# Optimization experiments

Hardware: AMD Instinct MI355X
Metric: run time of the kernel (lower is better)

The kernel has to match this reference:

```python
import jax, jax.numpy as jnp
import numpy as np

MAX_K = 16
CLUSTER_ITERS = 3
TEMP = 0.8
EPS = 1e-6


def setup_inputs() -> dict:
    key = jax.random.key(0)
    k1, k2 = jax.random.split(key, 2)
    B, C, H, W = 4, 256, 128, 128
    embeddings = jax.random.normal(k1, (B, C, H, W), dtype=jnp.float32)
    # 1x1 conv == per-pixel linear: weight [max_k, C], bias [max_k]
    seed_w = jax.random.normal(k2, (MAX_K, C), dtype=jnp.float32) * 0.05
    seed_b = jnp.zeros((MAX_K,), dtype=jnp.float32)
    return {"embeddings": embeddings, "seed_w": seed_w, "seed_b": seed_b, "k": 8}


def reference(embeddings, seed_w, seed_b, k):
    b, c, h, w = embeddings.shape
    n = h * w
    feats = embeddings.reshape(b, c, n)                     # [b,c,n]

    # seed_proj (1x1 conv) restricted to first k output channels
    seeds = jnp.einsum('oc,bcn->bon', seed_w[:k], feats) + seed_b[:k][None, :, None]
    assign = jax.nn.softmax(seeds, axis=1)                  # [b,k,n]
    proto = jnp.einsum('bkn,bcn->bkc', assign, feats) / (assign.sum(axis=2)[..., None] + EPS)

    # ||f||^2 is constant across iterations
    f_sq = jnp.sum(feats * feats, axis=1)                   # [b,n]

    logits = None
    for _ in range(CLUSTER_ITERS):                          # small fixed iter count
        p_sq = jnp.sum(proto * proto, axis=2)               # [b,k]
        cross = jnp.einsum('bkc,bcn->bkn', proto, feats)    # [b,k,n]
        # squared L2 distance via matmul trick (same math as (f-p)^2 sum over c)
        dist = f_sq[:, None, :] + p_sq[:, :, None] - 2.0 * cross
        logits = -dist / TEMP                               # [b,k,n]
        assign = jax.nn.softmax(logits, axis=1)
        denom = assign.sum(axis=2, keepdims=True) + EPS     # [b,k,1]
        proto = jnp.einsum('bkn,bcn->bkc', assign, feats) / denom

    logits_map = logits.reshape(b, k, h, w)
    probs = jax.nn.softmax(logits_map, axis=1)
    # bilinear upsample x4, align_corners=False (half-pixel) == jax 'linear' resize
    probs_full = jax.image.resize(probs, (b, k, 4 * h, 4 * w), method='linear')
    return probs_full, proto, logits_map
```

## Files before the change

kernel.cpp:

```cpp
#include <hip/hip_runtime.h>
#include <hip/hip_bf16.h>
#include <math.h>

#define BB   4
#define CCH  256
#define KK   8
#define NPIX 16384
#define TILE 64
#define NBLK 256
#define TEMP_INV 1.25f
#define EPSF 1e-6f

__device__ __forceinline__ float bf_lo(unsigned int u) { return __uint_as_float(u << 16); }
__device__ __forceinline__ float bf_hi(unsigned int u) { return __uint_as_float(u & 0xffff0000u); }

template<int MODE>
__global__ __launch_bounds__(512, 6)
void skm_pass(const float* __restrict__ feats,
              const float* __restrict__ seed_w,
              const float* __restrict__ seed_b,
              const float* __restrict__ proto_t,
              const float* __restrict__ psq_ws,
              float* __restrict__ fsq,
              float* __restrict__ part_num,
              float* __restrict__ part_den,
              float* __restrict__ logits_out,
              float* __restrict__ probs_out)
{
    __shared__ unsigned int fb_s[CCH][32];
    __shared__ float cross_s[8][KK][66];
    __shared__ float w_s[KK][68];
    __shared__ float aux_s[8][TILE];

    const int t   = threadIdx.x;
    const int bid = blockIdx.x;
    const int b   = bid >> 8;
    const int blk = bid & 255;
    const int n0  = blk * TILE;

    const int p  = t & 63;
    const int g  = t >> 6;
    const int c0 = __builtin_amdgcn_readfirstlane(g) * 32;
    const float* fcol = feats + (size_t)b * CCH * NPIX + (size_t)c0 * NPIX + n0 + p;
    const float* pt   = proto_t + (size_t)b * CCH * KK + (size_t)c0 * KK;

    float cr[KK];
    #pragma unroll
    for (int k = 0; k < KK; ++k) cr[k] = 0.f;
    float fs = 0.f;

    #pragma unroll 8
    for (int cc = 0; cc < 32; ++cc) {
        const float f = fcol[(size_t)cc * NPIX];
        if (MODE == 0) fs = fmaf(f, f, fs);
        const int c  = c0 + cc;
        const int wp = (p >> 1) ^ ((c & 15) << 1);
        ((__hip_bfloat16*)fb_s)[(c << 6) + (wp << 1) + (p & 1)] = __float2bfloat16(f);
        if (MODE == 0) {
            #pragma unroll
            for (int k = 0; k < KK; ++k)
                cr[k] = fmaf(seed_w[k * CCH + c], f, cr[k]);
        } else {
            const float* pr = pt + cc * KK;
            #pragma unroll
            for (int k = 0; k < KK; ++k)
                cr[k] = fmaf(pr[k], f, cr[k]);
        }
    }
    #pragma unroll
    for (int k = 0; k < KK; ++k) cross_s[g][k][p] = cr[k];
    if (MODE == 0) aux_s[g][p] = fs;
    __syncthreads();

    {
        const int pp = t >> 3, k = t & 7;
        float lg = 0.f;
        #pragma unroll
        for (int gg = 0; gg < 8; ++gg) lg += cross_s[gg][k][pp];
        if (MODE == 0) {
            lg += seed_b[k];
            if (k == 0) {
                float fv = 0.f;
                #pragma unroll
                for (int gg = 0; gg < 8; ++gg) fv += aux_s[gg][pp];
                fsq[b * NPIX + n0 + pp] = fv;
            }
        } else {
            const float fv = fsq[b * NPIX + n0 + pp];
            const float pk = psq_ws[b * KK + k];
            lg = (2.f * lg - fv - pk) * TEMP_INV;
        }
        float m = lg;
        m = fmaxf(m, __shfl_xor(m, 1, 64));
        m = fmaxf(m, __shfl_xor(m, 2, 64));
        m = fmaxf(m, __shfl_xor(m, 4, 64));
        const float e = expf(lg - m);
        float ssum = e;
        ssum += __shfl_xor(ssum, 1, 64);
        ssum += __shfl_xor(ssum, 2, 64);
        ssum += __shfl_xor(ssum, 4, 64);
        const float wv = e / ssum;
        w_s[k][pp] = wv;
        if (MODE == 2) aux_s[k][pp] = lg;
    }
    __syncthreads();

    if (MODE == 2) {
        const int k2 = t >> 6, p2 = t & 63;
        logits_out[((size_t)b * KK + k2) * NPIX + n0 + p2] = aux_s[k2][p2];
        probs_out [((size_t)b * KK + k2) * NPIX + n0 + p2] = w_s[k2][p2];
    }

    if (t < 256) {
        const int kk = t >> 5, l = t & 31;
        float s = w_s[kk][2 * l] + w_s[kk][2 * l + 1];
        s += __shfl_xor(s, 16, 64);
        s += __shfl_xor(s, 8, 64);
        s += __shfl_xor(s, 4, 64);
        s += __shfl_xor(s, 2, 64);
        s += __shfl_xor(s, 1, 64);
        if (l == 0) part_den[(b * NBLK + blk) * KK + kk] = s;
    }

    {
        const int c = t & 255, h = t >> 8;
        const int s2 = (c & 15) << 1;
        const uint2* row2 = (const uint2*)fb_s[c];
        float acc[KK];
        #pragma unroll
        for (int k = 0; k < KK; ++k) acc[k] = 0.f;
        #pragma unroll
        for (int j = 0; j < 8; ++j) {
            const uint2 u = row2[((16 * h + 2 * j) ^ s2) >> 1];
            const float f0 = bf_lo(u.x), f1 = bf_hi(u.x);
            const float f2 = bf_lo(u.y), f3 = bf_hi(u.y);
            const int px = 32 * h + 4 * j;
            #pragma unroll
            for (int k = 0; k < KK; ++k) {
                const float4 w4 = *(const float4*)&w_s[k][px];
                acc[k] = fmaf(f3, w4.w, fmaf(f2, w4.z,
                         fmaf(f1, w4.y, fmaf(f0, w4.x, acc[k]))));
            }
        }
        float (*acc_s)[KK][CCH] = (float (*)[KK][CCH])cross_s;
        #pragma unroll
        for (int k = 0; k < KK; ++k) acc_s[h][k][c] = acc[k];
        __syncthreads();
        #pragma unroll
        for (int u2 = t; u2 < KK * CCH; u2 += 512) {
            const int k = u2 >> 8, c2 = u2 & 255;
            part_num[(((size_t)b * NBLK + blk) * KK + k) * CCH + c2] =
                acc_s[0][k][c2] + acc_s[1][k][c2];
        }
    }
}

__global__ __launch_bounds__(1024)
void skm_reduce(const float* __restrict__ part_num,
                const float* __restrict__ part_den,
                float* __restrict__ proto_t,
                float* __restrict__ psq_ws,
                float* __restrict__ proto_out)
{
    const int bid = blockIdx.x;
    const int b = bid >> 3, k = bid & 7;
    const int t = threadIdx.x;
    const int jj = t >> 8, c = t & 255;

    float s = 0.f;
    #pragma unroll 8
    for (int j = 0; j < 64; ++j)
        s += part_num[(((size_t)b * NBLK + jj * 64 + j) * KK + k) * CCH + c];

    __shared__ float red_s[4][CCH];
    __shared__ float den4[4];
    __shared__ float red2[CCH];
    red_s[jj][c] = s;

    if (t < 256) {
        float dv = part_den[(b * NBLK + t) * KK + k];
        dv += __shfl_xor(dv, 32, 64);
        dv += __shfl_xor(dv, 16, 64);
        dv += __shfl_xor(dv, 8, 64);
        dv += __shfl_xor(dv, 4, 64);
        dv += __shfl_xor(dv, 2, 64);
        dv += __shfl_xor(dv, 1, 64);
        if ((t & 63) == 0) den4[t >> 6] = dv;
    }
    __syncthreads();

    if (t < 256) {
        const float den = den4[0] + den4[1] + den4[2] + den4[3] + EPSF;
        const float pv = (red_s[0][t] + red_s[1][t] + red_s[2][t] + red_s[3][t]) / den;
        proto_t[((size_t)b * CCH + t) * KK + k] = pv;
        if (proto_out) proto_out[(b * KK + k) * CCH + t] = pv;
        red2[t] = pv * pv;
    }
    __syncthreads();
    if (t < 64) {
        float v = red2[t] + red2[t + 64] + red2[t + 128] + red2[t + 192];
        v += __shfl_xor(v, 32, 64);
        v += __shfl_xor(v, 16, 64);
        v += __shfl_xor(v, 8, 64);
        v += __shfl_xor(v, 4, 64);
        v += __shfl_xor(v, 2, 64);
        v += __shfl_xor(v, 1, 64);
        if (t == 0) psq_ws[b * KK + k] = v;
    }
}

__global__ __launch_bounds__(256)
void skm_upsample(const float* __restrict__ probs, float* __restrict__ outp)
{
    const int gid = blockIdx.x * 256 + threadIdx.x;
    const int jb = gid & 127;
    const int i  = (gid >> 7) & 511;
    const int bk = gid >> 16;
    const float* src = probs + (size_t)bk * NPIX;

    const float y   = i * 0.25f - 0.375f;
    const float y0f = floorf(y);
    const float fy  = y - y0f;
    const int   y0  = (int)y0f;
    const int ya = min(max(y0, 0), 127);
    const int yb = min(max(y0 + 1, 0), 127);
    const int xm = max(jb - 1, 0);
    const int xp = min(jb + 1, 127);

    const float* r0 = src + ya * 128;
    const float* r1 = src + yb * 128;
    const float wy0 = 1.f - fy;
    const float am = r0[xm] * wy0 + r1[xm] * fy;
    const float ac = r0[jb] * wy0 + r1[jb] * fy;
    const float ap = r0[xp] * wy0 + r1[xp] * fy;

    float4 o;
    o.x = 0.375f * am + 0.625f * ac;
    o.y = 0.125f * am + 0.875f * ac;
    o.z = 0.875f * ac + 0.125f * ap;
    o.w = 0.625f * ac + 0.375f * ap;
    ((float4*)outp)[gid] = o;
}

extern "C" void kernel_launch(void* const* d_in, const int* in_sizes, int n_in,
                              void* d_out, int out_size, void* d_ws, size_t ws_size,
                              hipStream_t stream)
{
    const float* feats  = (const float*)d_in[0];
    const float* seed_w = (const float*)d_in[1];
    const float* seed_b = (const float*)d_in[2];

    float* out        = (float*)d_out;
    float* probs_full = out;
    float* proto_out  = out + 8388608;
    float* logits_out = out + 8388608 + 8192;

    float* part_num = probs_full;

    float* ws       = (float*)d_ws;
    float* fsq      = ws;
    float* part_den = ws + 65536;
    float* proto_t  = part_den + 8192;
    float* psq_ws   = proto_t + 8192;
    float* probs_ws = psq_ws + 32;

    const dim3 pg(BB * NBLK), pb(512);
    const dim3 rg(32), rb(1024);

    skm_pass<0><<<pg, pb, 0, stream>>>(feats, seed_w, seed_b, proto_t, psq_ws,
                                       fsq, part_num, part_den, nullptr, nullptr);
    skm_reduce<<<rg, rb, 0, stream>>>(part_num, part_den, proto_t, psq_ws, nullptr);
    skm_pass<1><<<pg, pb, 0, stream>>>(feats, seed_w, seed_b, proto_t, psq_ws,
                                       fsq, part_num, part_den, nullptr, nullptr);
    skm_reduce<<<rg, rb, 0, stream>>>(part_num, part_den, proto_t, psq_ws, nullptr);
    skm_pass<1><<<pg, pb, 0, stream>>>(feats, seed_w, seed_b, proto_t, psq_ws,
                                       fsq, part_num, part_den, nullptr, nullptr);
    skm_reduce<<<rg, rb, 0, stream>>>(part_num, part_den, proto_t, psq_ws, nullptr);
    skm_pass<2><<<pg, pb, 0, stream>>>(feats, seed_w, seed_b, proto_t, psq_ws,
                                       fsq, part_num, part_den, logits_out, probs_ws);
    skm_reduce<<<rg, rb, 0, stream>>>(part_num, part_den, proto_t, psq_ws, proto_out);
    skm_upsample<<<dim3(8192), dim3(256), 0, stream>>>(probs_ws, probs_full);
}
```

Before: 109.6 us.

## Cache bf16 feature copy for later passes, split reduce, fuse upsample

The first pass writes a bf16 copy of the features to workspace, and later passes read it instead of the fp32 input, halving feature read traffic. The reduce kernel is split into 288 smaller blocks per (batch, cluster), with channel slices reduced separately. The final reduce launch also carries the upsample blocks, removing one launch. The cost is an extra 32MB write in pass 0 and bf16 rounding of the cross-term in later iterations, which changes numerics. It also needs a large workspace and falls back to the old path otherwise.

New measurement: 177.5 us. +62.0%, slower.

```diff
diff --git a/kernel.cpp b/kernel.cpp
--- a/kernel.cpp
+++ b/kernel.cpp
@@ -11,10 +11,12 @@
 #define TEMP_INV 1.25f
 #define EPSF 1e-6f
 
+typedef unsigned short ushort_t;
+
 __device__ __forceinline__ float bf_lo(unsigned int u) { return __uint_as_float(u << 16); }
 __device__ __forceinline__ float bf_hi(unsigned int u) { return __uint_as_float(u & 0xffff0000u); }
 
-template<int MODE>
+template<int MODE, int BF>
 __global__ __launch_bounds__(512, 6)
 void skm_pass(const float* __restrict__ feats,
               const float* __restrict__ seed_w,
@@ -25,7 +27,8 @@
               float* __restrict__ part_num,
               float* __restrict__ part_den,
               float* __restrict__ logits_out,
-              float* __restrict__ probs_out)
+              float* __restrict__ probs_out,
+              __hip_bfloat16* __restrict__ feats_bf)
 {
     __shared__ unsigned int fb_s[CCH][32];
     __shared__ float cross_s[8][KK][66];
@@ -38,38 +41,65 @@
     const int blk = bid & 255;
     const int n0  = blk * TILE;
 
-    const int p  = t & 63;
-    const int g  = t >> 6;
-    const int c0 = __builtin_amdgcn_readfirstlane(g) * 32;
-    const float* fcol = feats + (size_t)b * CCH * NPIX + (size_t)c0 * NPIX + n0 + p;
-    const float* pt   = proto_t + (size_t)b * CCH * KK + (size_t)c0 * KK;
-
-    float cr[KK];
-    #pragma unroll
-    for (int k = 0; k < KK; ++k) cr[k] = 0.f;
-    float fs = 0.f;
-
-    #pragma unroll 8
-    for (int cc = 0; cc < 32; ++cc) {
-        const float f = fcol[(size_t)cc * NPIX];
-        if (MODE == 0) fs = fmaf(f, f, fs);
-        const int c  = c0 + cc;
-        const int wp = (p >> 1) ^ ((c & 15) << 1);
-        ((__hip_bfloat16*)fb_s)[(c << 6) + (wp << 1) + (p & 1)] = __float2bfloat16(f);
-        if (MODE == 0) {
-            #pragma unroll
-            for (int k = 0; k < KK; ++k)
-                cr[k] = fmaf(seed_w[k * CCH + c], f, cr[k]);
-        } else {
+    const int l   = t & 63;
+    const int g   = t >> 6;
+    const int c0g = __builtin_amdgcn_readfirstlane(g) * 32;
+
+    if (MODE == 0 || !BF) {
+        const int p = l;
+        const float* fcol = feats + (size_t)b * CCH * NPIX + (size_t)c0g * NPIX + n0 + p;
+        const float* pt   = proto_t + (size_t)b * CCH * KK + (size_t)c0g * KK;
+        float cr[KK];
+        #pragma unroll
+        for (int k = 0; k < KK; ++k) cr[k] = 0.f;
+        float fs = 0.f;
+        #pragma unroll 8
+        for (int cc = 0; cc < 32; ++cc) {
+            const float f = fcol[(size_t)cc * NPIX];
+            if (MODE == 0) fs = fmaf(f, f, fs);
+            const int c  = c0g + cc;
+            const int wp = (p >> 1) ^ ((c & 15) << 1);
+            const __hip_bfloat16 hv = __float2bfloat16(f);
+            ((__hip_bfloat16*)fb_s)[(c << 6) + (wp << 1) + (p & 1)] = hv;
+            if (MODE == 0 && BF)
+                feats_bf[(size_t)(b * CCH + c) * NPIX + n0 + p] = hv;
+            if (MODE == 0) {
+                #pragma unroll
+                for (int k = 0; k < KK; ++k)
+                    cr[k] = fmaf(seed_w[k * CCH + c], f, cr[k]);
+            } else {
+                const float* pr = pt + cc * KK;
+                #pragma unroll
+                for (int k = 0; k < KK; ++k)
+                    cr[k] = fmaf(pr[k], f, cr[k]);
+            }
+        }
+        #pragma unroll
+        for (int k = 0; k < KK; ++k) cross_s[g][k][p] = cr[k];
+        if (MODE == 0) aux_s[g][p] = fs;
+    } else {
+        const int wsel = l & 31;
+        const int sh   = (l < 32) ? 16 : 0;
+        const int p1   = 2 * wsel + (l >> 5);
+        const ushort_t* fbrow = (const ushort_t*)feats_bf
+                              + (size_t)(b * CCH + c0g) * NPIX + n0 + 2 * wsel;
+        const float* pt = proto_t + (size_t)b * CCH * KK + (size_t)c0g * KK;
+        float cr[KK];
+        #pragma unroll
+        for (int k = 0; k < KK; ++k) cr[k] = 0.f;
+        #pragma unroll 8
+        for (int cc = 0; cc < 32; ++cc) {
+            const unsigned int u = *(const unsigned int*)(fbrow + (size_t)cc * NPIX);
+            const float f = __uint_as_float((u << sh) & 0xffff0000u);
+            if (l < 32) fb_s[c0g + cc][wsel ^ ((cc & 15) << 1)] = u;
             const float* pr = pt + cc * KK;
             #pragma unroll
             for (int k = 0; k < KK; ++k)
                 cr[k] = fmaf(pr[k], f, cr[k]);
         }
-    }
-    #pragma unroll
-    for (int k = 0; k < KK; ++k) cross_s[g][k][p] = cr[k];
-    if (MODE == 0) aux_s[g][p] = fs;
+        #pragma unroll
+        for (int k = 0; k < KK; ++k) cross_s[g][k][p1] = cr[k];
+    }
     __syncthreads();
 
     {
@@ -112,14 +142,14 @@
     }
 
     if (t < 256) {
-        const int kk = t >> 5, l = t & 31;
-        float s = w_s[kk][2 * l] + w_s[kk][2 * l + 1];
+        const int kk = t >> 5, ll = t & 31;
+        float s = w_s[kk][2 * ll] + w_s[kk][2 * ll + 1];
         s += __shfl_xor(s, 16, 64);
         s += __shfl_xor(s, 8, 64);
         s += __shfl_xor(s, 4, 64);
         s += __shfl_xor(s, 2, 64);
         s += __shfl_xor(s, 1, 64);
-        if (l == 0) part_den[(b * NBLK + blk) * KK + kk] = s;
+        if (ll == 0) part_den[(b * NBLK + blk) * KK + kk] = s;
     }
 
     {
@@ -155,57 +185,104 @@
     }
 }
 
-__global__ __launch_bounds__(1024)
+template<bool FINAL>
+__global__ __launch_bounds__(256)
 void skm_reduce(const float* __restrict__ part_num,
                 const float* __restrict__ part_den,
                 float* __restrict__ proto_t,
                 float* __restrict__ psq_ws,
-                float* __restrict__ proto_out)
+                float* __restrict__ proto_out,
+                const float* __restrict__ probs_ws,
+                float* __restrict__ probs_full)
 {
     const int bid = blockIdx.x;
-    const int b = bid >> 3, k = bid & 7;
+    if (FINAL && bid >= 288) {
+        const int gid = (bid - 288) * 256 + threadIdx.x;
+        const int jb = gid & 127;
+        const int i  = (gid >> 7) & 511;
+        const int bk = gid >> 16;
+        const float* src = probs_ws + (size_t)bk * NPIX;
+        const float y   = i * 0.25f - 0.375f;
+        const float y0f = floorf(y);
+        const float fy  = y - y0f;
+        const int   y0  = (int)y0f;
+        const int ya = min(max(y0, 0), 127);
+        const int yb = min(max(y0 + 1, 0), 127);
+        const int xm = max(jb - 1, 0);
+        const int xp = min(jb + 1, 127);
+        const float* r0 = src + ya * 128;
+        const float* r1 = src + yb * 128;
+        const float wy0 = 1.f - fy;
+        const float am = r0[xm] * wy0 + r1[xm] * fy;
+        const float ac = r0[jb] * wy0 + r1[jb] * fy;
+        const float ap = r0[xp] * wy0 + r1[xp] * fy;
+        float4 o;
+        o.x = 0.375f * am + 0.625f * ac;
+        o.y = 0.125f * am + 0.875f * ac;
+        o.z = 0.875f * ac + 0.125f * ap;
+        o.w = 0.625f * ac + 0.375f * ap;
+        ((float4*)probs_full)[gid] = o;
+        return;
+    }
+
+    const int cq = bid % 9;
+    const int bk = bid / 9;
+    const int b = bk >> 3, k = bk & 7;
     const int t = threadIdx.x;
-    const int jj = t >> 8, c = t & 255;
-
-    float s = 0.f;
-    #pragma unroll 8
-    for (int j = 0; j < 64; ++j)
-        s += part_num[(((size_t)b * NBLK + jj * 64 + j) * KK + k) * CCH + c];
-
-    __shared__ float red_s[4][CCH];
-    __shared__ float den4[4];
-    __shared__ float red2[CCH];
-    red_s[jj][c] = s;
-
-    if (t < 256) {
-        float dv = part_den[(b * NBLK + t) * KK + k];
-        dv += __shfl_xor(dv, 32, 64);
-        dv += __shfl_xor(dv, 16, 64);
-        dv += __shfl_xor(dv, 8, 64);
-        dv += __shfl_xor(dv, 4, 64);
-        dv += __shfl_xor(dv, 2, 64);
-        dv += __shfl_xor(dv, 1, 64);
-        if ((t & 63) == 0) den4[t >> 6] = dv;
-    }
+
+    __shared__ float red[8][32];
+    __shared__ float den_s[4];
+    __shared__ float red2[256];
+
+    float dv = part_den[(b * NBLK + t) * KK + k];
+    dv += __shfl_xor(dv, 32, 64);
+    dv += __shfl_xor(dv, 16, 64);
+    dv += __shfl_xor(dv, 8, 64);
+    dv += __shfl_xor(dv, 4, 64);
+    dv += __shfl_xor(dv, 2, 64);
+    dv += __shfl_xor(dv, 1, 64);
+    if ((t & 63) == 0) den_s[t >> 6] = dv;
     __syncthreads();
-
-    if (t < 256) {
-        const float den = den4[0] + den4[1] + den4[2] + den4[3] + EPSF;
-        const float pv = (red_s[0][t] + red_s[1][t] + red_s[2][t] + red_s[3][t]) / den;
-        proto_t[((size_t)b * CCH + t) * KK + k] = pv;
-        if (proto_out) proto_out[(b * KK + k) * CCH + t] = pv;
+    const float den = den_s[0] + den_s[1] + den_s[2] + den_s[3] + EPSF;
+
+    if (cq < 8) {
+        const int jj = t >> 5, cl = t & 31;
+        const int c = cq * 32 + cl;
+        float s = 0.f;
+        #pragma unroll 4
+        for (int j = 0; j < 32; ++j)
+            s += part_num[(((size_t)b * NBLK + jj * 32 + j) * KK + k) * CCH + c];
+        red[jj][cl] = s;
+        __syncthreads();
+        if (t < 32) {
+            float pv = 0.f;
+            #pragma unroll
+            for (int j2 = 0; j2 < 8; ++j2) pv += red[j2][t];
+            pv /= den;
+            const int c2 = cq * 32 + t;
+            proto_t[((size_t)b * CCH + c2) * KK + k] = pv;
+            if (proto_out) proto_out[(b * KK + k) * CCH + c2] = pv;
+        }
+    } else {
+        float num = 0.f;
+        #pragma unroll 8
+        for (int j = 0; j < NBLK; ++j)
+            num += part_num[(((size_t)b * NBLK + j) * KK + k) * CCH + t];
+        const float pv = num / den;
         red2[t] = pv * pv;
-    }
-    __syncthreads();
-    if (t < 64) {
-        float v = red2[t] + red2[t + 64] + red2[t + 128] + red2[t + 192];
-        v += __shfl_xor(v, 32, 64);
-        v += __shfl_xor(v, 16, 64);
-        v += __shfl_xor(v, 8, 64);
-        v += __shfl_xor(v, 4, 64);
-        v += __shfl_xor(v, 2, 64);
-        v += __shfl_xor(v, 1, 64);
-        if (t == 0) psq_ws[b * KK + k] = v;
+        __syncthreads();
+        if (t < 128) red2[t] += red2[t + 128];
+        __syncthreads();
+        if (t < 64) {
+            float v = red2[t] + red2[t + 64];
+            v += __shfl_xor(v, 32, 64);
+            v += __shfl_xor(v, 16, 64);
+            v += __shfl_xor(v, 8, 64);
+            v += __shfl_xor(v, 4, 64);
+            v += __shfl_xor(v, 2, 64);
+            v += __shfl_xor(v, 1, 64);
+            if (t == 0) psq_ws[b * KK + k] = v;
+        }
     }
 }
 
@@ -217,7 +294,6 @@
     const int i  = (gid >> 7) & 511;
     const int bk = gid >> 16;
     const float* src = probs + (size_t)bk * NPIX;
-
     const float y   = i * 0.25f - 0.375f;
     const float y0f = floorf(y);
     const float fy  = y - y0f;
@@ -226,14 +302,12 @@
     const int yb = min(max(y0 + 1, 0), 127);
     const int xm = max(jb - 1, 0);
     const int xp = min(jb + 1, 127);
-
     const float* r0 = src + ya * 128;
     const float* r1 = src + yb * 128;
     const float wy0 = 1.f - fy;
     const float am = r0[xm] * wy0 + r1[xm] * fy;
     const float ac = r0[jb] * wy0 + r1[jb] * fy;
     const float ap = r0[xp] * wy0 + r1[xp] * fy;
-
     float4 o;
     o.x = 0.375f * am + 0.625f * ac;
     o.y = 0.125f * am + 0.875f * ac;
@@ -255,8 +329,6 @@
     float* proto_out  = out + 8388608;
     float* logits_out = out + 8388608 + 8192;
 
-    float* part_num = probs_full;
-
     float* ws       = (float*)d_ws;
     float* fsq      = ws;
     float* part_den = ws + 65536;
@@ -264,20 +336,48 @@
     float* psq_ws   = proto_t + 8192;
     float* probs_ws = psq_ws + 32;
 
+    const bool big_ws = ws_size >= (size_t)45 * 1024 * 1024;
+    __hip_bfloat16* feats_bf = (__hip_bfloat16*)(ws + 606272);
+    float* part_num = big_ws ? (ws + 606272 + 16777216)
+                             : probs_full;
+
     const dim3 pg(BB * NBLK), pb(512);
-    const dim3 rg(32), rb(1024);
-
-    skm_pass<0><<<pg, pb, 0, stream>>>(feats, seed_w, seed_b, proto_t, psq_ws,
-                                       fsq, part_num, part_den, nullptr, nullptr);
-    skm_reduce<<<rg, rb, 0, stream>>>(part_num, part_den, proto_t, psq_ws, nullptr);
-    skm_pass<1><<<pg, pb, 0, stream>>>(feats, seed_w, seed_b, proto_t, psq_ws,
-                                       fsq, part_num, part_den, nullptr, nullptr);
-    skm_reduce<<<rg, rb, 0, stream>>>(part_num, part_den, proto_t, psq_ws, nullptr);
-    skm_pass<1><<<pg, pb, 0, stream>>>(feats, seed_w, seed_b, proto_t, psq_ws,
-                                       fsq, part_num, part_den, nullptr, nullptr);
-    skm_reduce<<<rg, rb, 0, stream>>>(part_num, part_den, proto_t, psq_ws, nullptr);
-    skm_pass<2><<<pg, pb, 0, stream>>>(feats, seed_w, seed_b, proto_t, psq_ws,
-                                       fsq, part_num, part_den, logits_out, probs_ws);
-    skm_reduce<<<rg, rb, 0, stream>>>(part_num, part_den, proto_t, psq_ws, proto_out);
-    skm_upsample<<<dim3(8192), dim3(256), 0, stream>>>(probs_ws, probs_full);
+    const dim3 rg(288), rb(256);
+
+    if (big_ws) {
+        skm_pass<0,1><<<pg, pb, 0, stream>>>(feats, seed_w, seed_b, proto_t, psq_ws,
+                                             fsq, part_num, part_den, nullptr, nullptr, feats_bf);
+        skm_reduce<false><<<rg, rb, 0, stream>>>(part_num, part_den, proto_t, psq_ws,
+                                                 nullptr, probs_ws, probs_full);
+        skm_pass<1,1><<<pg, pb, 0, stream>>>(feats, seed_w, seed_b, proto_t, psq_ws,
+                                             fsq, part_num, part_den, nullptr, nullptr, feats_bf);
+        skm_reduce<false><<<rg, rb, 0, stream>>>(part_num, part_den, proto_t, psq_ws,
+                                                 nullptr, probs_ws, probs_full);
+        skm_pass<1,1><<<pg, pb, 0, stream>>>(feats, seed_w, seed_b, proto_t, psq_ws,
+                                             fsq, part_num, part_den, nullptr, nullptr, feats_bf);
+        skm_reduce<false><<<rg, rb, 0, stream>>>(part_num, part_den, proto_t, psq_ws,
+                                                 nullptr, probs_ws, probs_full);
+        skm_pass<2,1><<<pg, pb, 0, stream>>>(feats, seed_w, seed_b, proto_t, psq_ws,
+                                             fsq, part_num, part_den, logits_out, probs_ws, feats_bf);
+        skm_reduce<true><<<dim3(288 + 8192), rb, 0, stream>>>(part_num, part_den, proto_t, psq_ws,
+                                                              proto_out, probs_ws, probs_full);
+    } else {
+        skm_pass<0,0><<<pg, pb, 0, stream>>>(feats, seed_w, seed_b, proto_t, psq_ws,
+                                             fsq, part_num, part_den, nullptr, nullptr, nullptr);
+        skm_reduce<false><<<rg, rb, 0, stream>>>(part_num, part_den, proto_t, psq_ws,
+                                                 nullptr, probs_ws, probs_full);
+        skm_pass<1,0><<<pg, pb, 0, stream>>>(feats, seed_w, seed_b, proto_t, psq_ws,
+                                             fsq, part_num, part_den, nullptr, nullptr, nullptr);
+        skm_reduce<false><<<rg, rb, 0, stream>>>(part_num, part_den, proto_t, psq_ws,
+                                                 nullptr, probs_ws, probs_full);
+        skm_pass<1,0><<<pg, pb, 0, stream>>>(feats, seed_w, seed_b, proto_t, psq_ws,
+                                             fsq, part_num, part_den, nullptr, nullptr, nullptr);
+        skm_reduce<false><<<rg, rb, 0, stream>>>(part_num, part_den, proto_t, psq_ws,
+                                                 nullptr, probs_ws, probs_full);
+        skm_pass<2,0><<<pg, pb, 0, stream>>>(feats, seed_w, seed_b, proto_t, psq_ws,
+                                             fsq, part_num, part_den, logits_out, probs_ws, nullptr);
+        skm_reduce<false><<<rg, rb, 0, stream>>>(part_num, part_den, proto_t, psq_ws,
+                                                 proto_out, probs_ws, probs_full);
+        skm_upsample<<<dim3(8192), dim3(256), 0, stream>>>(probs_ws, probs_full);
+    }
 }
```

## Split prototype reduction across more blocks and fuse upsample into final reduce

Applied to the files above, without the earlier changes.

The prototype reduction now runs as 288 blocks of 256 threads instead of 32 blocks of 1024. Each (b,k) gets eight channel-slice blocks plus one block that recomputes the full sum only to get the squared prototype norm, which spreads the partial-sum reads over more CUs. The final reduce launch also carries the bilinear upsample blocks, removing one kernel launch. Partial numerators move from the output buffer into workspace, which is needed because the upsample now writes the output concurrently. The price is duplicated reading of partials by the norm blocks.

Result: slower. 140.1 us (+27.9%).

```diff
diff --git a/kernel.cpp b/kernel.cpp
--- a/kernel.cpp
+++ b/kernel.cpp
@@ -112,14 +112,14 @@
     }
 
     if (t < 256) {
-        const int kk = t >> 5, l = t & 31;
-        float s = w_s[kk][2 * l] + w_s[kk][2 * l + 1];
+        const int kk = t >> 5, ll = t & 31;
+        float s = w_s[kk][2 * ll] + w_s[kk][2 * ll + 1];
         s += __shfl_xor(s, 16, 64);
         s += __shfl_xor(s, 8, 64);
         s += __shfl_xor(s, 4, 64);
         s += __shfl_xor(s, 2, 64);
         s += __shfl_xor(s, 1, 64);
-        if (l == 0) part_den[(b * NBLK + blk) * KK + kk] = s;
+        if (ll == 0) part_den[(b * NBLK + blk) * KK + kk] = s;
     }
 
     {
@@ -155,91 +155,105 @@
     }
 }
 
-__global__ __launch_bounds__(1024)
+template<bool FINAL>
+__global__ __launch_bounds__(256)
 void skm_reduce(const float* __restrict__ part_num,
                 const float* __restrict__ part_den,
                 float* __restrict__ proto_t,
                 float* __restrict__ psq_ws,
-                float* __restrict__ proto_out)
+                float* __restrict__ proto_out,
+                const float* __restrict__ probs_ws,
+                float* __restrict__ probs_full)
 {
     const int bid = blockIdx.x;
-    const int b = bid >> 3, k = bid & 7;
+    if (FINAL && bid >= 288) {
+        const int gid = (bid - 288) * 256 + threadIdx.x;
+        const int jb = gid & 127;
+        const int i  = (gid >> 7) & 511;
+        const int bk = gid >> 16;
+        const float* src = probs_ws + (size_t)bk * NPIX;
+        const float y   = i * 0.25f - 0.375f;
+        const float y0f = floorf(y);
+        const float fy  = y - y0f;
+        const int   y0  = (int)y0f;
+        const int ya = min(max(y0, 0), 127);
+        const int yb = min(max(y0 + 1, 0), 127);
+        const int xm = max(jb - 1, 0);
+        const int xp = min(jb + 1, 127);
+        const float* r0 = src + ya * 128;
+        const float* r1 = src + yb * 128;
+        const float wy0 = 1.f - fy;
+        const float am = r0[xm] * wy0 + r1[xm] * fy;
+        const float ac = r0[jb] * wy0 + r1[jb] * fy;
+        const float ap = r0[xp] * wy0 + r1[xp] * fy;
+        float4 o;
+        o.x = 0.375f * am + 0.625f * ac;
+        o.y = 0.125f * am + 0.875f * ac;
+        o.z = 0.875f * ac + 0.125f * ap;
+        o.w = 0.625f * ac + 0.375f * ap;
+        ((float4*)probs_full)[gid] = o;
+        return;
+    }
+
+    const int cq = bid % 9;
+    const int bk = bid / 9;
+    const int b = bk >> 3, k = bk & 7;
     const int t = threadIdx.x;
-    const int jj = t >> 8, c = t & 255;
-
-    float s = 0.f;
-    #pragma unroll 8
-    for (int j = 0; j < 64; ++j)
-        s += part_num[(((size_t)b * NBLK + jj * 64 + j) * KK + k) * CCH + c];
-
-    __shared__ float red_s[4][CCH];
-    __shared__ float den4[4];
-    __shared__ float red2[CCH];
-    red_s[jj][c] = s;
-
-    if (t < 256) {
-        float dv = part_den[(b * NBLK + t) * KK + k];
-        dv += __shfl_xor(dv, 32, 64);
-        dv += __shfl_xor(dv, 16, 64);
-        dv += __shfl_xor(dv, 8, 64);
-        dv += __shfl_xor(dv, 4, 64);
-        dv += __shfl_xor(dv, 2, 64);
-        dv += __shfl_xor(dv, 1, 64);
-        if ((t & 63) == 0) den4[t >> 6] = dv;
-    }
+
+    __shared__ float red[8][32];
+    __shared__ float den_s[4];
+    __shared__ float red2[256];
+
+    float dv = part_den[(b * NBLK + t) * KK + k];
+    dv += __shfl_xor(dv, 32, 64);
+    dv += __shfl_xor(dv, 16, 64);
+    dv += __shfl_xor(dv, 8, 64);
+    dv += __shfl_xor(dv, 4, 64);
+    dv += __shfl_xor(dv, 2, 64);
+    dv += __shfl_xor(dv, 1, 64);
+    if ((t & 63) == 0) den_s[t >> 6] = dv;
     __syncthreads();
-
-    if (t < 256) {
-        const float den = den4[0] + den4[1] + den4[2] + den4[3] + EPSF;
-        const float pv = (red_s[0][t] + red_s[1][t] + red_s[2][t] + red_s[3][t]) / den;
-        proto_t[((size_t)b * CCH + t) * KK + k] = pv;
-        if (proto_out) proto_out[(b * KK + k) * CCH + t] = pv;
+    const float den = den_s[0] + den_s[1] + den_s[2] + den_s[3] + EPSF;
+
+    if (cq < 8) {
+        const int jj = t >> 5, cl = t & 31;
+        const int c = cq * 32 + cl;
+        float s = 0.f;
+        #pragma unroll 4
+        for (int j = 0; j < 32; ++j)
+            s += part_num[(((size_t)b * NBLK + jj * 32 + j) * KK + k) * CCH + c];
+        red[jj][cl] = s;
+        __syncthreads();
+        if (t < 32) {
+            float pv = 0.f;
+            #pragma unroll
+            for (int j2 = 0; j2 < 8; ++j2) pv += red[j2][t];
+            pv /= den;
+            const int c2 = cq * 32 + t;
+            proto_t[((size_t)b * CCH + c2) * KK + k] = pv;
+            if (proto_out) proto_out[(b * KK + k) * CCH + c2] = pv;
+        }
+    } else {
+        float num = 0.f;
+        #pragma unroll 8
+        for (int j = 0; j < NBLK; ++j)
+            num += part_num[(((size_t)b * NBLK + j) * KK + k) * CCH + t];
+        const float pv = num / den;
         red2[t] = pv * pv;
-    }
-    __syncthreads();
-    if (t < 64) {
-        float v = red2[t] + red2[t + 64] + red2[t + 128] + red2[t + 192];
-        v += __shfl_xor(v, 32, 64);
-        v += __shfl_xor(v, 16, 64);
-        v += __shfl_xor(v, 8, 64);
-        v += __shfl_xor(v, 4, 64);
-        v += __shfl_xor(v, 2, 64);
-        v += __shfl_xor(v, 1, 64);
-        if (t == 0) psq_ws[b * KK + k] = v;
-    }
-}
-
-__global__ __launch_bounds__(256)
-void skm_upsample(const float* __restrict__ probs, float* __restrict__ outp)
-{
-    const int gid = blockIdx.x * 256 + threadIdx.x;
-    const int jb = gid & 127;
-    const int i  = (gid >> 7) & 511;
-    const int bk = gid >> 16;
-    const float* src = probs + (size_t)bk * NPIX;
-
-    const float y   = i * 0.25f - 0.375f;
-    const float y0f = floorf(y);
-    const float fy  = y - y0f;
-    const int   y0  = (int)y0f;
-    const int ya = min(max(y0, 0), 127);
-    const int yb = min(max(y0 + 1, 0), 127);
-    const int xm = max(jb - 1, 0);
-    const int xp = min(jb + 1, 127);
-
-    const float* r0 = src + ya * 128;
-    const float* r1 = src + yb * 128;
-    const float wy0 = 1.f - fy;
-    const float am = r0[xm] * wy0 + r1[xm] * fy;
-    const float ac = r0[jb] * wy0 + r1[jb] * fy;
-    const float ap = r0[xp] * wy0 + r1[xp] * fy;
-
-    float4 o;
-    o.x = 0.375f * am + 0.625f * ac;
-    o.y = 0.125f * am + 0.875f * ac;
-    o.z = 0.875f * ac + 0.125f * ap;
-    o.w = 0.625f * ac + 0.375f * ap;
-    ((float4*)outp)[gid] = o;
+        __syncthreads();
+        if (t < 128) red2[t] += red2[t + 128];
+        __syncthreads();
+        if (t < 64) {
+            float v = red2[t] + red2[t + 64];
+            v += __shfl_xor(v, 32, 64);
+            v += __shfl_xor(v, 16, 64);
+            v += __shfl_xor(v, 8, 64);
+            v += __shfl_xor(v, 4, 64);
+            v += __shfl_xor(v, 2, 64);
+            v += __shfl_xor(v, 1, 64);
+            if (t == 0) psq_ws[b * KK + k] = v;
+        }
+    }
 }
 
 extern "C" void kernel_launch(void* const* d_in, const int* in_sizes, int n_in,
@@ -255,29 +269,31 @@
     float* proto_out  = out + 8388608;
     float* logits_out = out + 8388608 + 8192;
 
-    float* part_num = probs_full;
-
     float* ws       = (float*)d_ws;
     float* fsq      = ws;
     float* part_den = ws + 65536;
     float* proto_t  = part_den + 8192;
     float* psq_ws   = proto_t + 8192;
     float* probs_ws = psq_ws + 32;
+    float* part_num = probs_ws + 524288;
 
     const dim3 pg(BB * NBLK), pb(512);
-    const dim3 rg(32), rb(1024);
+    const dim3 rg(288), rb(256);
 
     skm_pass<0><<<pg, pb, 0, stream>>>(feats, seed_w, seed_b, proto_t, psq_ws,
                                        fsq, part_num, part_den, nullptr, nullptr);
-    skm_reduce<<<rg, rb, 0, stream>>>(part_num, part_den, proto_t, psq_ws, nullptr);
+    skm_reduce<false><<<rg, rb, 0, stream>>>(part_num, part_den, proto_t, psq_ws,
+                                             nullptr, probs_ws, probs_full);
     skm_pass<1><<<pg, pb, 0, stream>>>(feats, seed_w, seed_b, proto_t, psq_ws,
                                        fsq, part_num, part_den, nullptr, nullptr);
-    skm_reduce<<<rg, rb, 0, stream>>>(part_num, part_den, proto_t, psq_ws, nullptr);
+    skm_reduce<false><<<rg, rb, 0, stream>>>(part_num, part_den, proto_t, psq_ws,
+                                             nullptr, probs_ws, probs_full);
     skm_pass<1><<<pg, pb, 0, stream>>>(feats, seed_w, seed_b, proto_t, psq_ws,
                                        fsq, part_num, part_den, nullptr, nullptr);
-    skm_reduce<<<rg, rb, 0, stream>>>(part_num, part_den, proto_t, psq_ws, nullptr);
+    skm_reduce<false><<<rg, rb, 0, stream>>>(part_num, part_den, proto_t, psq_ws,
+                                             nullptr, probs_ws, probs_full);
     skm_pass<2><<<pg, pb, 0, stream>>>(feats, seed_w, seed_b, proto_t, psq_ws,
                                        fsq, part_num, part_den, logits_out, probs_ws);
-    skm_reduce<<<rg, rb, 0, stream>>>(part_num, part_den, proto_t, psq_ws, proto_out);
-    skm_upsample<<<dim3(8192), dim3(256), 0, stream>>>(probs_ws, probs_full);
+    skm_reduce<true><<<dim3(288 + 8192), rb, 0, stream>>>(part_num, part_den, proto_t, psq_ws,
+                                                          proto_out, probs_ws, probs_full);
 }
```
